# Optimization experiments

Measured on AMD Instinct MI355X. Metric: run time of the kernel, lower is better.

## Reference

```python
import jax, jax.numpy as jnp
import numpy as np

ALPHA = 0.2    # LeakyReLU negative slope (init arg alpha)
HEADS = 8
EPS = 1e-5     # LayerNorm eps


def setup_inputs() -> dict:
    key = jax.random.key(0)
    ks = jax.random.split(key, 16)
    B, S, D = 4, 1024, 256
    dh = D // HEADS  # 32
    x = jax.random.normal(ks[0], (B, S, D), jnp.float32)
    adj = (jax.random.uniform(ks[1], (B, S, S)) < 0.05).astype(jnp.float32)
    adj = jnp.maximum(adj, jnp.eye(S, dtype=jnp.float32)[None])

    def w(k, shape, fan):
        return jax.random.normal(k, shape, jnp.float32) * (fan ** -0.5)

    # GAT layer 0: in->hidden (concat heads)
    W0 = w(ks[2], (D, D), D); a_src0 = w(ks[3], (HEADS, dh), dh); a_dst0 = w(ks[4], (HEADS, dh), dh)
    # GAT layer 1: hidden->hidden (concat heads)
    W1 = w(ks[5], (D, D), D); a_src1 = w(ks[6], (HEADS, dh), dh); a_dst1 = w(ks[7], (HEADS, dh), dh)
    # GAT layer 2: hidden->out (mean over heads, head_dim = out_dim)
    W2 = w(ks[8], (D, HEADS * D), D); a_src2 = w(ks[9], (HEADS, D), D); a_dst2 = w(ks[10], (HEADS, D), D)
    # LayerNorm
    ln_g = jnp.ones((D,), jnp.float32); ln_b = jnp.zeros((D,), jnp.float32)
    # FFN: D -> 2D -> D
    ff_w1 = w(ks[11], (D, 2 * D), D); ff_b1 = jnp.zeros((2 * D,), jnp.float32)
    ff_w2 = w(ks[12], (2 * D, D), 2 * D); ff_b2 = jnp.zeros((D,), jnp.float32)
    return dict(adj=adj, x=x, W0=W0, a_src0=a_src0, a_dst0=a_dst0,
                W1=W1, a_src1=a_src1, a_dst1=a_dst1,
                W2=W2, a_src2=a_src2, a_dst2=a_dst2,
                ln_g=ln_g, ln_b=ln_b,
                ff_w1=ff_w1, ff_b1=ff_b1, ff_w2=ff_w2, ff_b2=ff_b2)


def _gat_layer(h, adj, W, a_src, a_dst, concat):
    B, S, _ = h.shape
    hp = jnp.einsum('bsi,io->bso', h, W).reshape(B, S, HEADS, -1)  # [B,S,H,dh]
    src = jnp.einsum('bshd,hd->bsh', hp, a_src)  # per-node source score
    dst = jnp.einsum('bshd,hd->bsh', hp, a_dst)  # per-node dest score
    # e[b,i,j,h] = LeakyReLU(src_i + dst_j), masked by adjacency
    e = jax.nn.leaky_relu(src[:, :, None, :] + dst[:, None, :, :], ALPHA)
    e = jnp.where(adj[..., None] > 0, e, jnp.float32(-1e9))
    attn = jax.nn.softmax(e, axis=2)  # softmax over neighbors j
    out = jnp.einsum('bijh,bjhd->bihd', attn, hp)
    return out.reshape(B, S, -1) if concat else out.mean(axis=2)


def reference(adj, x, W0, a_src0, a_dst0, W1, a_src1, a_dst1, W2, a_src2, a_dst2,
              ln_g, ln_b, ff_w1, ff_b1, ff_w2, ff_b2):
    # MultiAttentionGAT: 3 layers with residuals, ELU between layers
    h = jax.nn.elu(_gat_layer(x, adj, W0, a_src0, a_dst0, True) + x)
    h = jax.nn.elu(_gat_layer(h, adj, W1, a_src1, a_dst1, True) + h)
    h = _gat_layer(h, adj, W2, a_src2, a_dst2, False) + h
    # LayerNorm
    mu = h.mean(-1, keepdims=True)
    var = h.var(-1, keepdims=True)
    h = (h - mu) * jax.lax.rsqrt(var + EPS) * ln_g + ln_b
    # GELU FFN + residual
    ff = jnp.dot(jax.nn.gelu(jnp.dot(h, ff_w1) + ff_b1), ff_w2) + ff_b2
    return h + ff
```

## Files before the change

### kernel.cpp

```cpp
#include <hip/hip_runtime.h>
#include <hip/hip_bf16.h>

#define B_ 4
#define S_ 1024
#define D_ 256
#define H_ 8
#define LRELU_ALPHA 0.2f
#define MAXDEG 128

typedef __attribute__((ext_vector_type(8))) short short8;
typedef __attribute__((ext_vector_type(4))) float floatx4;

__device__ __forceinline__ float bf2f(unsigned short u) {
    union { unsigned int i; float f; } c; c.i = ((unsigned int)u) << 16; return c.f;
}
__device__ __forceinline__ unsigned short f2bf(float f) {
    union { float f; unsigned int u; } c; c.f = f;
    unsigned int r = (c.u + 0x7FFF + ((c.u >> 16) & 1)) >> 16;
    return (unsigned short)r;
}

__device__ void castT_body(const float* __restrict__ W, unsigned short* __restrict__ out,
                           int K, int N, int k0, int n0, float (*t)[33], int tid) {
    int tx = tid & 31, ty = tid >> 5;
#pragma unroll
    for (int i = 0; i < 4; ++i)
        t[ty + 8 * i][tx] = W[(size_t)(k0 + ty + 8 * i) * N + n0 + tx];
    __syncthreads();
#pragma unroll
    for (int i = 0; i < 4; ++i)
        out[(size_t)(n0 + ty + 8 * i) * K + k0 + tx] = f2bf(t[tx][ty + 8 * i]);
}

__global__ __launch_bounds__(256) void k_prep(
        const float* __restrict__ x, unsigned short* __restrict__ xb,
        const float* __restrict__ W0, unsigned short* __restrict__ W0t,
        const float* __restrict__ W1, unsigned short* __restrict__ W1t,
        const float* __restrict__ W2, unsigned short* __restrict__ W2t,
        const float* __restrict__ F1, unsigned short* __restrict__ F1t,
        const float* __restrict__ F2, unsigned short* __restrict__ F2t,
        const float* __restrict__ as2, const float* __restrict__ ad2,
        float* __restrict__ WS2, float* __restrict__ WD2,
        const float* __restrict__ adj, int* __restrict__ nbr, int* __restrict__ cnt) {
    __shared__ float t[32][33];
    __shared__ int c;
    int b = blockIdx.x, tid = threadIdx.x;
    if (b < 1024) {
        int i = b * 256 + tid;
        float4 v = ((const float4*)x)[i];
        ushort4 u; u.x = f2bf(v.x); u.y = f2bf(v.y); u.z = f2bf(v.z); u.w = f2bf(v.w);
        ((ushort4*)xb)[i] = u;
    } else if (b < 1088) {
        int i = b - 1024; castT_body(W0, W0t, 256, 256, (i & 7) * 32, (i >> 3) * 32, t, tid);
    } else if (b < 1152) {
        int i = b - 1088; castT_body(W1, W1t, 256, 256, (i & 7) * 32, (i >> 3) * 32, t, tid);
    } else if (b < 1664) {
        int i = b - 1152;
        int k0 = (i & 7) * 32, d0 = ((i >> 3) & 7) * 32, h = i >> 6;
        int tx = tid & 31, ty = tid >> 5;
#pragma unroll
        for (int q = 0; q < 4; ++q)
            t[ty + 8 * q][tx] = W2[(size_t)(k0 + ty + 8 * q) * 2048 + h * 256 + d0 + tx];
        __syncthreads();
#pragma unroll
        for (int q = 0; q < 4; ++q)
            W2t[(size_t)(d0 + ty + 8 * q) * 2048 + h * 256 + k0 + tx] = f2bf(t[tx][ty + 8 * q]);
    } else if (b < 1792) {
        int i = b - 1664; castT_body(F1, F1t, 256, 512, (i & 7) * 32, (i >> 3) * 32, t, tid);
    } else if (b < 1920) {
        int i = b - 1792; castT_body(F2, F2t, 512, 256, (i & 15) * 32, (i >> 4) * 32, t, tid);
    } else if (b < 2432) {
        int id = (b - 1920) * 4 + (tid >> 6);
        int h = id >> 8, k = id & 255;
        int lane = tid & 63;
        float4 w4 = *(const float4*)(W2 + (size_t)k * 2048 + h * 256 + lane * 4);
        float4 a4 = *(const float4*)(as2 + h * 256 + lane * 4);
        float4 d4 = *(const float4*)(ad2 + h * 256 + lane * 4);
        float s = w4.x * a4.x + w4.y * a4.y + w4.z * a4.z + w4.w * a4.w;
        float d = w4.x * d4.x + w4.y * d4.y + w4.z * d4.z + w4.w * d4.w;
#pragma unroll
        for (int o = 32; o; o >>= 1) { s += __shfl_xor(s, o); d += __shfl_xor(d, o); }
        if (lane == 0) { WS2[h * 256 + k] = s; WD2[h * 256 + k] = d; }
    } else {
        int row = b - 2432;
        if (tid == 0) c = 0;
        __syncthreads();
        float4 a4 = ((const float4*)(adj + (size_t)row * S_))[tid];
#pragma unroll
        for (int q = 0; q < 4; ++q) {
            float a = q == 0 ? a4.x : q == 1 ? a4.y : q == 2 ? a4.z : a4.w;
            if (a > 0.f) {
                int s = atomicAdd(&c, 1);
                if (s < MAXDEG) nbr[row * MAXDEG + s] = tid * 4 + q;
            }
        }
        __syncthreads();
        if (tid == 0) cnt[row] = c < MAXDEG ? c : MAXDEG;
    }
}

__global__ __launch_bounds__(256) void k_gemm_wide(const unsigned short* __restrict__ A,
        const unsigned short* __restrict__ Bt, float* __restrict__ P,
        int M, int N, int K, int Kc) {
    __shared__ unsigned short As[64][40];
    __shared__ unsigned short Bs[256][40];
    int tid = threadIdx.x;
    int bm = blockIdx.y * 64, bn = blockIdx.x * 256;
    int kbeg = blockIdx.z * Kc, kend = kbeg + Kc;
    int lane = tid & 63, wv = tid >> 6;
    int lrow = lane & 15, lq = lane >> 4;
    floatx4 acc[4][4] = {};
    int sm = tid >> 2, skq = (tid & 3) * 8;
    const unsigned short* Ap = A + (size_t)(bm + sm) * K + skq;
    const unsigned short* Bp0 = Bt + (size_t)(bn + sm) * K + skq;
    const unsigned short* Bp1 = Bp0 + (size_t)64 * K;
    const unsigned short* Bp2 = Bp0 + (size_t)128 * K;
    const unsigned short* Bp3 = Bp0 + (size_t)192 * K;
    short8 av  = *(const short8*)(Ap + kbeg);
    short8 bv0 = *(const short8*)(Bp0 + kbeg);
    short8 bv1 = *(const short8*)(Bp1 + kbeg);
    short8 bv2 = *(const short8*)(Bp2 + kbeg);
    short8 bv3 = *(const short8*)(Bp3 + kbeg);
    for (int k0 = kbeg; k0 < kend; k0 += 32) {
        *(short8*)&As[sm][skq]        = av;
        *(short8*)&Bs[sm][skq]        = bv0;
        *(short8*)&Bs[sm + 64][skq]   = bv1;
        *(short8*)&Bs[sm + 128][skq]  = bv2;
        *(short8*)&Bs[sm + 192][skq]  = bv3;
        __syncthreads();
        if (k0 + 32 < kend) {
            av  = *(const short8*)(Ap + k0 + 32);
            bv0 = *(const short8*)(Bp0 + k0 + 32);
            bv1 = *(const short8*)(Bp1 + k0 + 32);
            bv2 = *(const short8*)(Bp2 + k0 + 32);
            bv3 = *(const short8*)(Bp3 + k0 + 32);
        }
        short8 aF[4], bF[4];
#pragma unroll
        for (int mi = 0; mi < 4; ++mi)
            aF[mi] = *(const short8*)&As[mi * 16 + lrow][lq * 8];
#pragma unroll
        for (int ni = 0; ni < 4; ++ni)
            bF[ni] = *(const short8*)&Bs[wv * 64 + ni * 16 + lrow][lq * 8];
#pragma unroll
        for (int mi = 0; mi < 4; ++mi)
#pragma unroll
            for (int ni = 0; ni < 4; ++ni)
                acc[mi][ni] = __builtin_amdgcn_mfma_f32_16x16x32_bf16(aF[mi], bF[ni], acc[mi][ni], 0, 0, 0);
        __syncthreads();
    }
    float* out = P + (size_t)blockIdx.z * M * N;
#pragma unroll
    for (int mi = 0; mi < 4; ++mi)
#pragma unroll
        for (int ni = 0; ni < 4; ++ni)
#pragma unroll
            for (int r = 0; r < 4; ++r) {
                int grow = bm + mi * 16 + lq * 4 + r;
                int gcol = bn + wv * 64 + ni * 16 + lrow;
                out[(size_t)grow * N + gcol] = acc[mi][ni][r];
            }
}

__global__ __launch_bounds__(256) void k_gemm64s(
        const unsigned short* __restrict__ A, const unsigned short* __restrict__ Bt,
        int N, int K,
        unsigned short* __restrict__ Ob,
        const float* __restrict__ p1, const float* __restrict__ p2,
        float* __restrict__ SRC, float* __restrict__ DST) {
    __shared__ unsigned short As[2][64][40];
    __shared__ unsigned short Bs[2][64][40];
    int tid = threadIdx.x;
    int bm = blockIdx.y * 64, bn = blockIdx.x * 64;
    int lane = tid & 63, wv = tid >> 6;
    int lrow = lane & 15, lq = lane >> 4;
    floatx4 acc[4] = {};
    int sm = tid >> 2, skq = (tid & 3) * 8;
    const unsigned short* Ap = A + (size_t)(bm + sm) * K + skq;
    const unsigned short* Bp = Bt + (size_t)(bn + sm) * K + skq;
    short8 av = *(const short8*)Ap;
    short8 bv = *(const short8*)Bp;
    *(short8*)&As[0][sm][skq] = av;
    *(short8*)&Bs[0][sm][skq] = bv;
    __syncthreads();
    int cur = 0;
    for (int k0 = 0; k0 < K; k0 += 32) {
        bool more = k0 + 32 < K;
        if (more) {
            av = *(const short8*)(Ap + k0 + 32);
            bv = *(const short8*)(Bp + k0 + 32);
        }
        short8 aF = *(const short8*)&As[cur][wv * 16 + lrow][lq * 8];
        short8 bF[4];
#pragma unroll
        for (int ni = 0; ni < 4; ++ni)
            bF[ni] = *(const short8*)&Bs[cur][ni * 16 + lrow][lq * 8];
#pragma unroll
        for (int ni = 0; ni < 4; ++ni)
            acc[ni] = __builtin_amdgcn_mfma_f32_16x16x32_bf16(aF, bF[ni], acc[ni], 0, 0, 0);
        if (more) {
            *(short8*)&As[cur ^ 1][sm][skq] = av;
            *(short8*)&Bs[cur ^ 1][sm][skq] = bv;
            __syncthreads();
            cur ^= 1;
        }
    }
    int row0 = bm + wv * 16 + lq * 4;
#pragma unroll
    for (int ni = 0; ni < 4; ++ni)
#pragma unroll
        for (int r = 0; r < 4; ++r)
            Ob[(size_t)(row0 + r) * N + bn + ni * 16 + lrow] = f2bf(acc[ni][r]);
    float asv[4], adv[4];
#pragma unroll
    for (int ni = 0; ni < 4; ++ni) {
        asv[ni] = p1[bn + ni * 16 + lrow];
        adv[ni] = p2[bn + ni * 16 + lrow];
    }
#pragma unroll
    for (int r = 0; r < 4; ++r) {
        float sA = acc[0][r] * asv[0] + acc[1][r] * asv[1];
        float sB = acc[2][r] * asv[2] + acc[3][r] * asv[3];
        float dA = acc[0][r] * adv[0] + acc[1][r] * adv[1];
        float dB = acc[2][r] * adv[2] + acc[3][r] * adv[3];
#pragma unroll
        for (int o = 8; o; o >>= 1) {
            sA += __shfl_xor(sA, o); sB += __shfl_xor(sB, o);
            dA += __shfl_xor(dA, o); dB += __shfl_xor(dB, o);
        }
        if (lrow == 0) {
            int h0 = bn >> 5;
            SRC[(row0 + r) * 8 + h0]     = sA;
            SRC[(row0 + r) * 8 + h0 + 1] = sB;
            DST[(row0 + r) * 8 + h0]     = dA;
            DST[(row0 + r) * 8 + h0 + 1] = dB;
        }
    }
}

__global__ __launch_bounds__(256) void k_attn4(const unsigned short* __restrict__ hp,
        const float* __restrict__ src, const float* __restrict__ dst,
        const int* __restrict__ nbr, const int* __restrict__ cnts,
        const float* __restrict__ X, float* __restrict__ Hout,
        unsigned short* __restrict__ Hb,
        const float* __restrict__ WS2, const float* __restrict__ WD2,
        float* __restrict__ SRC2, float* __restrict__ DST2) {
    int tid = threadIdx.x;
    int rq = tid >> 6;
    int lane = tid & 63;
    int row = blockIdx.x * 4 + rq;
    int rb = row & ~(S_ - 1);
    __shared__ int nb[4][MAXDEG];
    __shared__ float ew[4][MAXDEG * 9];
    int cnt = cnts[row];
    for (int t = lane; t < cnt; t += 64) nb[rq][t] = nbr[row * MAXDEG + t];
    float4 sa = *(const float4*)(src + row * H_);
    float4 sb = *(const float4*)(src + row * H_ + 4);
    for (int n = lane; n < cnt; n += 64) {
        int j = nb[rq][n];
        const float* dp = dst + (size_t)(rb + j) * H_;
        float4 da = *(const float4*)dp;
        float4 db = *(const float4*)(dp + 4);
        float e;
        e = sa.x + da.x; ew[rq][n * 9 + 0] = e > 0.f ? e : LRELU_ALPHA * e;
        e = sa.y + da.y; ew[rq][n * 9 + 1] = e > 0.f ? e : LRELU_ALPHA * e;
        e = sa.z + da.z; ew[rq][n * 9 + 2] = e > 0.f ? e : LRELU_ALPHA * e;
        e = sa.w + da.w; ew[rq][n * 9 + 3] = e > 0.f ? e : LRELU_ALPHA * e;
        e = sb.x + db.x; ew[rq][n * 9 + 4] = e > 0.f ? e : LRELU_ALPHA * e;
        e = sb.y + db.y; ew[rq][n * 9 + 5] = e > 0.f ? e : LRELU_ALPHA * e;
        e = sb.z + db.z; ew[rq][n * 9 + 6] = e > 0.f ? e : LRELU_ALPHA * e;
        e = sb.w + db.w; ew[rq][n * 9 + 7] = e > 0.f ? e : LRELU_ALPHA * e;
    }
    {
        int h = lane >> 3, s8 = lane & 7;
        float m = -1e30f;
        for (int n = s8; n < cnt; n += 8) m = fmaxf(m, ew[rq][n * 9 + h]);
#pragma unroll
        for (int o = 4; o; o >>= 1) m = fmaxf(m, __shfl_xor(m, o));
        float s = 0.f;
        for (int n = s8; n < cnt; n += 8) {
            float v = __expf(ew[rq][n * 9 + h] - m); ew[rq][n * 9 + h] = v; s += v;
        }
#pragma unroll
        for (int o = 4; o; o >>= 1) s += __shfl_xor(s, o);
        float inv = s > 0.f ? 1.f / s : 0.f;
        for (int n = s8; n < cnt; n += 8) ew[rq][n * 9 + h] *= inv;
    }
    int d0 = lane * 4;
    int h = lane >> 3;
    const unsigned short* hpb = hp + (size_t)rb * 256 + d0;
    const float* ewr = ew[rq];
    float A0 = 0.f, A1 = 0.f, A2 = 0.f, A3 = 0.f;
    float B0 = 0.f, B1 = 0.f, B2 = 0.f, B3 = 0.f;
    int n = 0;
    for (; n + 3 < cnt; n += 4) {
        int j0 = nb[rq][n], j1 = nb[rq][n + 1];
        int j2 = nb[rq][n + 2], j3 = nb[rq][n + 3];
        uint2 p0 = *(const uint2*)(hpb + (size_t)j0 * 256);
        uint2 p1 = *(const uint2*)(hpb + (size_t)j1 * 256);
        uint2 p2 = *(const uint2*)(hpb + (size_t)j2 * 256);
        uint2 p3 = *(const uint2*)(hpb + (size_t)j3 * 256);
        float w0 = ewr[n * 9 + h], w1 = ewr[(n + 1) * 9 + h];
        float w2 = ewr[(n + 2) * 9 + h], w3 = ewr[(n + 3) * 9 + h];
        A0 += w0 * bf2f((unsigned short)p0.x); A1 += w0 * bf2f((unsigned short)(p0.x >> 16));
        A2 += w0 * bf2f((unsigned short)p0.y); A3 += w0 * bf2f((unsigned short)(p0.y >> 16));
        B0 += w1 * bf2f((unsigned short)p1.x); B1 += w1 * bf2f((unsigned short)(p1.x >> 16));
        B2 += w1 * bf2f((unsigned short)p1.y); B3 += w1 * bf2f((unsigned short)(p1.y >> 16));
        A0 += w2 * bf2f((unsigned short)p2.x); A1 += w2 * bf2f((unsigned short)(p2.x >> 16));
        A2 += w2 * bf2f((unsigned short)p2.y); A3 += w2 * bf2f((unsigned short)(p2.y >> 16));
        B0 += w3 * bf2f((unsigned short)p3.x); B1 += w3 * bf2f((unsigned short)(p3.x >> 16));
        B2 += w3 * bf2f((unsigned short)p3.y); B3 += w3 * bf2f((unsigned short)(p3.y >> 16));
    }
    for (; n < cnt; ++n) {
        int j = nb[rq][n];
        uint2 p = *(const uint2*)(hpb + (size_t)j * 256);
        float w = ewr[n * 9 + h];
        A0 += w * bf2f((unsigned short)p.x); A1 += w * bf2f((unsigned short)(p.x >> 16));
        A2 += w * bf2f((unsigned short)p.y); A3 += w * bf2f((unsigned short)(p.y >> 16));
    }
    float4 xv = *(const float4*)(X + (size_t)row * 256 + d0);
    float ov0 = A0 + B0 + xv.x;
    float ov1 = A1 + B1 + xv.y;
    float ov2 = A2 + B2 + xv.z;
    float ov3 = A3 + B3 + xv.w;
    ov0 = ov0 > 0.f ? ov0 : (__expf(ov0) - 1.f);
    ov1 = ov1 > 0.f ? ov1 : (__expf(ov1) - 1.f);
    ov2 = ov2 > 0.f ? ov2 : (__expf(ov2) - 1.f);
    ov3 = ov3 > 0.f ? ov3 : (__expf(ov3) - 1.f);
    *(float4*)(Hout + (size_t)row * 256 + d0) = make_float4(ov0, ov1, ov2, ov3);
    ushort4 ub; ub.x = f2bf(ov0); ub.y = f2bf(ov1); ub.z = f2bf(ov2); ub.w = f2bf(ov3);
    *(ushort4*)(Hb + (size_t)row * 256 + d0) = ub;
    if (WS2 != nullptr) {
#pragma unroll
        for (int hh = 0; hh < 8; ++hh) {
            float4 wsv = *(const float4*)(WS2 + hh * 256 + d0);
            float4 wdv = *(const float4*)(WD2 + hh * 256 + d0);
            float sP = ov0 * wsv.x + ov1 * wsv.y + ov2 * wsv.z + ov3 * wsv.w;
            float dP = ov0 * wdv.x + ov1 * wdv.y + ov2 * wdv.z + ov3 * wdv.w;
#pragma unroll
            for (int o = 32; o; o >>= 1) { sP += __shfl_xor(sP, o); dP += __shfl_xor(dP, o); }
            if (lane == 0) { SRC2[row * 8 + hh] = sP; DST2[row * 8 + hh] = dP; }
        }
    }
}

__global__ __launch_bounds__(256) void k_attn_Y(const unsigned short* __restrict__ Hb,
        const float* __restrict__ src2, const float* __restrict__ dst2,
        const int* __restrict__ nbr, const int* __restrict__ cnts,
        unsigned short* __restrict__ Ycat) {
    int tid = threadIdx.x;
    int half = tid >> 7, sub = tid & 127;
    int row = blockIdx.x * 2 + half;
    int rb = row & ~(S_ - 1);
    __shared__ int nb[2][MAXDEG];
    __shared__ float ew[2][MAXDEG * 8];
    int cnt = cnts[row];
    for (int t = sub; t < cnt; t += 128) nb[half][t] = nbr[row * MAXDEG + t];
    float4 sa = *(const float4*)(src2 + row * H_);
    float4 sb = *(const float4*)(src2 + row * H_ + 4);
    __syncthreads();
    for (int n = sub; n < cnt; n += 128) {
        int j = nb[half][n];
        const float* dp = dst2 + (size_t)(rb + j) * H_;
        float4 da = *(const float4*)dp;
        float4 db = *(const float4*)(dp + 4);
        float e;
        e = sa.x + da.x; ew[half][n * 8 + 0] = e > 0.f ? e : LRELU_ALPHA * e;
        e = sa.y + da.y; ew[half][n * 8 + 1] = e > 0.f ? e : LRELU_ALPHA * e;
        e = sa.z + da.z; ew[half][n * 8 + 2] = e > 0.f ? e : LRELU_ALPHA * e;
        e = sa.w + da.w; ew[half][n * 8 + 3] = e > 0.f ? e : LRELU_ALPHA * e;
        e = sb.x + db.x; ew[half][n * 8 + 4] = e > 0.f ? e : LRELU_ALPHA * e;
        e = sb.y + db.y; ew[half][n * 8 + 5] = e > 0.f ? e : LRELU_ALPHA * e;
        e = sb.z + db.z; ew[half][n * 8 + 6] = e > 0.f ? e : LRELU_ALPHA * e;
        e = sb.w + db.w; ew[half][n * 8 + 7] = e > 0.f ? e : LRELU_ALPHA * e;
    }
    __syncthreads();
    {
        int h = sub >> 4, s16 = sub & 15;
        float m = -1e30f;
        for (int n = s16; n < cnt; n += 16) m = fmaxf(m, ew[half][n * 8 + h]);
#pragma unroll
        for (int o = 8; o; o >>= 1) m = fmaxf(m, __shfl_xor(m, o));
        float s = 0.f;
        for (int n = s16; n < cnt; n += 16) {
            float v = __expf(ew[half][n * 8 + h] - m); ew[half][n * 8 + h] = v; s += v;
        }
#pragma unroll
        for (int o = 8; o; o >>= 1) s += __shfl_xor(s, o);
        float inv = s > 0.f ? 0.125f / s : 0.f;
        for (int n = s16; n < cnt; n += 16) ew[half][n * 8 + h] *= inv;
    }
    __syncthreads();
    const unsigned short* hbase = Hb + (size_t)rb * 256 + 2 * sub;
    const float* ewh = ew[half];
    float aA[8] = {}, aB[8] = {};
    int n = 0;
    for (; n + 1 < cnt; n += 2) {
        int j0 = nb[half][n], j1 = nb[half][n + 1];
        unsigned int p0 = *(const unsigned int*)(hbase + (size_t)j0 * 256);
        unsigned int p1 = *(const unsigned int*)(hbase + (size_t)j1 * 256);
        float4 w0a = *(const float4*)(ewh + n * 8);
        float4 w0b = *(const float4*)(ewh + n * 8 + 4);
        float4 w1a = *(const float4*)(ewh + (n + 1) * 8);
        float4 w1b = *(const float4*)(ewh + (n + 1) * 8 + 4);
        float v0a = bf2f((unsigned short)p0), v0b = bf2f((unsigned short)(p0 >> 16));
        float v1a = bf2f((unsigned short)p1), v1b = bf2f((unsigned short)(p1 >> 16));
        aA[0] += w0a.x * v0a + w1a.x * v1a;  aB[0] += w0a.x * v0b + w1a.x * v1b;
        aA[1] += w0a.y * v0a + w1a.y * v1a;  aB[1] += w0a.y * v0b + w1a.y * v1b;
        aA[2] += w0a.z * v0a + w1a.z * v1a;  aB[2] += w0a.z * v0b + w1a.z * v1b;
        aA[3] += w0a.w * v0a + w1a.w * v1a;  aB[3] += w0a.w * v0b + w1a.w * v1b;
        aA[4] += w0b.x * v0a + w1b.x * v1a;  aB[4] += w0b.x * v0b + w1b.x * v1b;
        aA[5] += w0b.y * v0a + w1b.y * v1a;  aB[5] += w0b.y * v0b + w1b.y * v1b;
        aA[6] += w0b.z * v0a + w1b.z * v1a;  aB[6] += w0b.z * v0b + w1b.z * v1b;
        aA[7] += w0b.w * v0a + w1b.w * v1a;  aB[7] += w0b.w * v0b + w1b.w * v1b;
    }
    for (; n < cnt; ++n) {
        int j = nb[half][n];
        unsigned int p = *(const unsigned int*)(hbase + (size_t)j * 256);
        float4 wa = *(const float4*)(ewh + n * 8);
        float4 wb = *(const float4*)(ewh + n * 8 + 4);
        float va = bf2f((unsigned short)p), vb = bf2f((unsigned short)(p >> 16));
        aA[0] += wa.x * va; aB[0] += wa.x * vb;
        aA[1] += wa.y * va; aB[1] += wa.y * vb;
        aA[2] += wa.z * va; aB[2] += wa.z * vb;
        aA[3] += wa.w * va; aB[3] += wa.w * vb;
        aA[4] += wb.x * va; aB[4] += wb.x * vb;
        aA[5] += wb.y * va; aB[5] += wb.y * vb;
        aA[6] += wb.z * va; aB[6] += wb.z * vb;
        aA[7] += wb.w * va; aB[7] += wb.w * vb;
    }
    unsigned short* yb = Ycat + (size_t)row * 2048 + 2 * sub;
#pragma unroll
    for (int hh = 0; hh < 8; ++hh) {
        ushort2 u; u.x = f2bf(aA[hh]); u.y = f2bf(aB[hh]);
        *(ushort2*)(yb + hh * 256) = u;
    }
}

__global__ __launch_bounds__(512) void k_tail3(
        const float* __restrict__ PP, const float* __restrict__ Hres,
        const float* __restrict__ g, const float* __restrict__ bta,
        const unsigned short* __restrict__ F1t, const float* __restrict__ b1,
        const unsigned short* __restrict__ F2t, const float* __restrict__ b2,
        float* __restrict__ out) {
    __shared__ unsigned short alnb[16][264];
    __shared__ unsigned short mid[16][520];
    __shared__ unsigned short Bs[2][256][36];
    int tid = threadIdx.x;
    int lane = tid & 63, wv = tid >> 6;
    int lrow = lane & 15, lq = lane >> 4;
    int r0 = blockIdx.x * 16;

    float4 gg = ((const float4*)g)[lane];
    float4 bbv = ((const float4*)bta)[lane];
#pragma unroll
    for (int pass = 0; pass < 2; ++pass) {
        int lr = wv * 2 + pass;
        int row = r0 + lr;
        float4 v = ((const float4*)(Hres + (size_t)row * 256))[lane];
#pragma unroll
        for (int sp = 0; sp < 8; ++sp) {
            float4 p = ((const float4*)(PP + (size_t)sp * 1048576 + (size_t)row * 256))[lane];
            v.x += p.x; v.y += p.y; v.z += p.z; v.w += p.w;
        }
        float s = v.x + v.y + v.z + v.w;
        float q = v.x * v.x + v.y * v.y + v.z * v.z + v.w * v.w;
#pragma unroll
        for (int o = 32; o; o >>= 1) { s += __shfl_xor(s, o); q += __shfl_xor(q, o); }
        float mu = s * (1.f / 256.f);
        float var = q * (1.f / 256.f) - mu * mu;
        if (var < 0.f) var = 0.f;
        float rs = rsqrtf(var + 1e-5f);
        ushort4 ub;
        ub.x = f2bf((v.x - mu) * rs * gg.x + bbv.x);
        ub.y = f2bf((v.y - mu) * rs * gg.y + bbv.y);
        ub.z = f2bf((v.z - mu) * rs * gg.z + bbv.z);
        ub.w = f2bf((v.w - mu) * rs * gg.w + bbv.w);
        *(ushort4*)&alnb[lr][lane * 4] = ub;
    }
    __syncthreads();

    int sm = tid >> 1, skq = (tid & 1) * 16;
    int colb = wv * 32 + lrow;

#pragma unroll 1
    for (int hf = 0; hf < 2; ++hf) {
        floatx4 acc1[2] = {};
        const unsigned short* Fp = F1t + (size_t)(hf * 256 + sm) * 256 + skq;
        short8 rb0 = *(const short8*)Fp;
        short8 rb1 = *(const short8*)(Fp + 8);
        __syncthreads();
        *(short8*)&Bs[0][sm][skq]     = rb0;
        *(short8*)&Bs[0][sm][skq + 8] = rb1;
        __syncthreads();
        int cur = 0;
        for (int st = 0; st < 8; ++st) {
            bool more = st < 7;
            if (more) {
                rb0 = *(const short8*)(Fp + (st + 1) * 32);
                rb1 = *(const short8*)(Fp + (st + 1) * 32 + 8);
            }
            int k0 = st * 32;
            short8 aF  = *(const short8*)&alnb[lrow][k0 + lq * 8];
            short8 bF0 = *(const short8*)&Bs[cur][wv * 32 + lrow][lq * 8];
            short8 bF1 = *(const short8*)&Bs[cur][wv * 32 + 16 + lrow][lq * 8];
            acc1[0] = __builtin_amdgcn_mfma_f32_16x16x32_bf16(aF, bF0, acc1[0], 0, 0, 0);
            acc1[1] = __builtin_amdgcn_mfma_f32_16x16x32_bf16(aF, bF1, acc1[1], 0, 0, 0);
            if (more) {
                *(short8*)&Bs[cur ^ 1][sm][skq]     = rb0;
                *(short8*)&Bs[cur ^ 1][sm][skq + 8] = rb1;
                __syncthreads();
                cur ^= 1;
            }
        }
#pragma unroll
        for (int ni = 0; ni < 2; ++ni) {
            int gcol = hf * 256 + colb + ni * 16;
            float bb = b1[gcol];
#pragma unroll
            for (int r = 0; r < 4; ++r) {
                float xx = acc1[ni][r] + bb;
                float tt = tanhf(0.7978845608028654f * (xx + 0.044715f * xx * xx * xx));
                mid[lq * 4 + r][gcol] = f2bf(0.5f * xx * (1.f + tt));
            }
        }
    }
    __syncthreads();

    floatx4 acc2[2] = {};
    const unsigned short* F2p = F2t + (size_t)sm * 512 + skq;
    short8 rc0 = *(const short8*)F2p;
    short8 rc1 = *(const short8*)(F2p + 8);
    *(short8*)&Bs[0][sm][skq]     = rc0;
    *(short8*)&Bs[0][sm][skq + 8] = rc1;
    __syncthreads();
    int cur = 0;
    for (int st = 0; st < 16; ++st) {
        bool more = st < 15;
        if (more) {
            rc0 = *(const short8*)(F2p + (st + 1) * 32);
            rc1 = *(const short8*)(F2p + (st + 1) * 32 + 8);
        }
        int k0 = st * 32;
        short8 aF  = *(const short8*)&mid[lrow][k0 + lq * 8];
        short8 bF0 = *(const short8*)&Bs[cur][wv * 32 + lrow][lq * 8];
        short8 bF1 = *(const short8*)&Bs[cur][wv * 32 + 16 + lrow][lq * 8];
        acc2[0] = __builtin_amdgcn_mfma_f32_16x16x32_bf16(aF, bF0, acc2[0], 0, 0, 0);
        acc2[1] = __builtin_amdgcn_mfma_f32_16x16x32_bf16(aF, bF1, acc2[1], 0, 0, 0);
        if (more) {
            *(short8*)&Bs[cur ^ 1][sm][skq]     = rc0;
            *(short8*)&Bs[cur ^ 1][sm][skq + 8] = rc1;
            __syncthreads();
            cur ^= 1;
        }
    }
#pragma unroll
    for (int ni = 0; ni < 2; ++ni) {
        int col = colb + ni * 16;
        float bb = b2[col];
#pragma unroll
        for (int r = 0; r < 4; ++r) {
            int lr = lq * 4 + r;
            float res = bf2f(alnb[lr][col]);
            out[(size_t)(r0 + lr) * 256 + col] = acc2[ni][r] + bb + res;
        }
    }
}

extern "C" void kernel_launch(void* const* d_in, const int* in_sizes, int n_in,
                              void* d_out, int out_size, void* d_ws, size_t ws_size,
                              hipStream_t stream) {
    const float* adj   = (const float*)d_in[0];
    const float* x     = (const float*)d_in[1];
    const float* W0    = (const float*)d_in[2];
    const float* as0   = (const float*)d_in[3];
    const float* ad0   = (const float*)d_in[4];
    const float* W1    = (const float*)d_in[5];
    const float* as1   = (const float*)d_in[6];
    const float* ad1   = (const float*)d_in[7];
    const float* W2    = (const float*)d_in[8];
    const float* as2   = (const float*)d_in[9];
    const float* ad2   = (const float*)d_in[10];
    const float* ln_g  = (const float*)d_in[11];
    const float* ln_b  = (const float*)d_in[12];
    const float* ff_w1 = (const float*)d_in[13];
    const float* ff_b1 = (const float*)d_in[14];
    const float* ff_w2 = (const float*)d_in[15];
    const float* ff_b2 = (const float*)d_in[16];

    float* ws = (float*)d_ws;
    float* H    = ws;
    unsigned short* Ycat = (unsigned short*)(ws + 2097152);
    unsigned short* HPb  = (unsigned short*)(ws + 6291456);
    unsigned short* xb   = (unsigned short*)(ws + 6815744);
    unsigned short* Hb   = (unsigned short*)(ws + 7340032);
    unsigned short* W0t  = (unsigned short*)(ws + 9437184);
    unsigned short* W1t  = (unsigned short*)(ws + 9469952);
    unsigned short* W2t  = (unsigned short*)(ws + 9502720);
    unsigned short* F1t  = (unsigned short*)(ws + 9764864);
    unsigned short* F2t  = (unsigned short*)(ws + 9830400);
    float* WS2  = ws + 9895936;
    float* WD2  = ws + 9897984;
    float* SRC  = ws + 9900032;
    float* DST  = ws + 9932800;
    float* SRC2 = ws + 9965568;
    float* DST2 = ws + 9998336;
    int*   NBR  = (int*)(ws + 10031104);
    int*   CNT  = (int*)(ws + 10555392);
    float* PP   = ws + 12582912;

    k_prep<<<6528, 256, 0, stream>>>(x, xb, W0, W0t, W1, W1t, W2, W2t,
                                     ff_w1, F1t, ff_w2, F2t, as2, ad2, WS2, WD2,
                                     adj, NBR, CNT);

    k_gemm64s<<<dim3(4, 64), 256, 0, stream>>>(xb, W0t, 256, 256, HPb, as0, ad0, SRC, DST);
    k_attn4<<<1024, 256, 0, stream>>>(HPb, SRC, DST, NBR, CNT, x, H, Hb,
                                      nullptr, nullptr, nullptr, nullptr);

    k_gemm64s<<<dim3(4, 64), 256, 0, stream>>>(Hb, W1t, 256, 256, HPb, as1, ad1, SRC, DST);
    k_attn4<<<1024, 256, 0, stream>>>(HPb, SRC, DST, NBR, CNT, H, H, Hb,
                                      WS2, WD2, SRC2, DST2);

    k_attn_Y<<<2048, 256, 0, stream>>>(Hb, SRC2, DST2, NBR, CNT, Ycat);
    k_gemm_wide<<<dim3(1, 64, 8), 256, 0, stream>>>(Ycat, W2t, PP, 4096, 256, 2048, 256);

    k_tail3<<<256, 512, 0, stream>>>(PP, H, ln_g, ln_b, F1t, ff_b1, F2t, ff_b2,
                                     (float*)d_out);
}
```

Baseline: 209.5 us.

## Double-buffer LDS in wide GEMM and split neighbor gather across half-waves

The wide GEMM now keeps two LDS stages, so the next K-slice is stored into the alternate buffer after the MFMAs. This drops one barrier per iteration and overlaps the global loads with compute, at the cost of doubling shared memory per block. The attention aggregation kernel now has each lane gather 8 bf16 values (16-byte loads), with the two half-waves handling alternating neighbors and combining partial sums by shuffle. This widens memory transactions and adds memory-level parallelism per row, but only half the lanes do the output writes.

```diff
diff --git a/kernel.cpp b/kernel.cpp
--- a/kernel.cpp
+++ b/kernel.cpp
@@ -102,8 +102,8 @@
 __global__ __launch_bounds__(256) void k_gemm_wide(const unsigned short* __restrict__ A,
         const unsigned short* __restrict__ Bt, float* __restrict__ P,
         int M, int N, int K, int Kc) {
-    __shared__ unsigned short As[64][40];
-    __shared__ unsigned short Bs[256][40];
+    __shared__ unsigned short As[2][64][40];
+    __shared__ unsigned short Bs[2][256][40];
     int tid = threadIdx.x;
     int bm = blockIdx.y * 64, bn = blockIdx.x * 256;
     int kbeg = blockIdx.z * Kc, kend = kbeg + Kc;
@@ -121,14 +121,16 @@
     short8 bv1 = *(const short8*)(Bp1 + kbeg);
     short8 bv2 = *(const short8*)(Bp2 + kbeg);
     short8 bv3 = *(const short8*)(Bp3 + kbeg);
+    *(short8*)&As[0][sm][skq]        = av;
+    *(short8*)&Bs[0][sm][skq]        = bv0;
+    *(short8*)&Bs[0][sm + 64][skq]   = bv1;
+    *(short8*)&Bs[0][sm + 128][skq]  = bv2;
+    *(short8*)&Bs[0][sm + 192][skq]  = bv3;
+    __syncthreads();
+    int cur = 0;
     for (int k0 = kbeg; k0 < kend; k0 += 32) {
-        *(short8*)&As[sm][skq]        = av;
-        *(short8*)&Bs[sm][skq]        = bv0;
-        *(short8*)&Bs[sm + 64][skq]   = bv1;
-        *(short8*)&Bs[sm + 128][skq]  = bv2;
-        *(short8*)&Bs[sm + 192][skq]  = bv3;
-        __syncthreads();
-        if (k0 + 32 < kend) {
+        bool more = k0 + 32 < kend;
+        if (more) {
             av  = *(const short8*)(Ap + k0 + 32);
             bv0 = *(const short8*)(Bp0 + k0 + 32);
             bv1 = *(const short8*)(Bp1 + k0 + 32);
@@ -138,16 +140,24 @@
         short8 aF[4], bF[4];
 #pragma unroll
         for (int mi = 0; mi < 4; ++mi)
-            aF[mi] = *(const short8*)&As[mi * 16 + lrow][lq * 8];
+            aF[mi] = *(const short8*)&As[cur][mi * 16 + lrow][lq * 8];
 #pragma unroll
         for (int ni = 0; ni < 4; ++ni)
-            bF[ni] = *(const short8*)&Bs[wv * 64 + ni * 16 + lrow][lq * 8];
+            bF[ni] = *(const short8*)&Bs[cur][wv * 64 + ni * 16 + lrow][lq * 8];
 #pragma unroll
         for (int mi = 0; mi < 4; ++mi)
 #pragma unroll
             for (int ni = 0; ni < 4; ++ni)
                 acc[mi][ni] = __builtin_amdgcn_mfma_f32_16x16x32_bf16(aF[mi], bF[ni], acc[mi][ni], 0, 0, 0);
-        __syncthreads();
+        if (more) {
+            *(short8*)&As[cur ^ 1][sm][skq]        = av;
+            *(short8*)&Bs[cur ^ 1][sm][skq]        = bv0;
+            *(short8*)&Bs[cur ^ 1][sm + 64][skq]   = bv1;
+            *(short8*)&Bs[cur ^ 1][sm + 128][skq]  = bv2;
+            *(short8*)&Bs[cur ^ 1][sm + 192][skq]  = bv3;
+            __syncthreads();
+            cur ^= 1;
+        }
     }
     float* out = P + (size_t)blockIdx.z * M * N;
 #pragma unroll
@@ -286,57 +296,70 @@
         float inv = s > 0.f ? 1.f / s : 0.f;
         for (int n = s8; n < cnt; n += 8) ew[rq][n * 9 + h] *= inv;
     }
-    int d0 = lane * 4;
-    int h = lane >> 3;
+    int half = lane >> 5, sl = lane & 31;
+    int d0 = sl * 8;
+    int h = sl >> 2;
     const unsigned short* hpb = hp + (size_t)rb * 256 + d0;
     const float* ewr = ew[rq];
-    float A0 = 0.f, A1 = 0.f, A2 = 0.f, A3 = 0.f;
-    float B0 = 0.f, B1 = 0.f, B2 = 0.f, B3 = 0.f;
-    int n = 0;
-    for (; n + 3 < cnt; n += 4) {
-        int j0 = nb[rq][n], j1 = nb[rq][n + 1];
-        int j2 = nb[rq][n + 2], j3 = nb[rq][n + 3];
-        uint2 p0 = *(const uint2*)(hpb + (size_t)j0 * 256);
-        uint2 p1 = *(const uint2*)(hpb + (size_t)j1 * 256);
-        uint2 p2 = *(const uint2*)(hpb + (size_t)j2 * 256);
-        uint2 p3 = *(const uint2*)(hpb + (size_t)j3 * 256);
-        float w0 = ewr[n * 9 + h], w1 = ewr[(n + 1) * 9 + h];
-        float w2 = ewr[(n + 2) * 9 + h], w3 = ewr[(n + 3) * 9 + h];
-        A0 += w0 * bf2f((unsigned short)p0.x); A1 += w0 * bf2f((unsigned short)(p0.x >> 16));
-        A2 += w0 * bf2f((unsigned short)p0.y); A3 += w0 * bf2f((unsigned short)(p0.y >> 16));
-        B0 += w1 * bf2f((unsigned short)p1.x); B1 += w1 * bf2f((unsigned short)(p1.x >> 16));
-        B2 += w1 * bf2f((unsigned short)p1.y); B3 += w1 * bf2f((unsigned short)(p1.y >> 16));
-        A0 += w2 * bf2f((unsigned short)p2.x); A1 += w2 * bf2f((unsigned short)(p2.x >> 16));
-        A2 += w2 * bf2f((unsigned short)p2.y); A3 += w2 * bf2f((unsigned short)(p2.y >> 16));
-        B0 += w3 * bf2f((unsigned short)p3.x); B1 += w3 * bf2f((unsigned short)(p3.x >> 16));
-        B2 += w3 * bf2f((unsigned short)p3.y); B3 += w3 * bf2f((unsigned short)(p3.y >> 16));
-    }
-    for (; n < cnt; ++n) {
+    float aA[8] = {}, aB[8] = {};
+    int n = half;
+    for (; n + 2 < cnt; n += 4) {
+        int j0 = nb[rq][n], j1 = nb[rq][n + 2];
+        uint4 p0 = *(const uint4*)(hpb + (size_t)j0 * 256);
+        uint4 p1 = *(const uint4*)(hpb + (size_t)j1 * 256);
+        float w0 = ewr[n * 9 + h], w1 = ewr[(n + 2) * 9 + h];
+        aA[0] += w0 * bf2f((unsigned short)p0.x); aA[1] += w0 * bf2f((unsigned short)(p0.x >> 16));
+        aA[2] += w0 * bf2f((unsigned short)p0.y); aA[3] += w0 * bf2f((unsigned short)(p0.y >> 16));
+        aA[4] += w0 * bf2f((unsigned short)p0.z); aA[5] += w0 * bf2f((unsigned short)(p0.z >> 16));
+        aA[6] += w0 * bf2f((unsigned short)p0.w); aA[7] += w0 * bf2f((unsigned short)(p0.w >> 16));
+        aB[0] += w1 * bf2f((unsigned short)p1.x); aB[1] += w1 * bf2f((unsigned short)(p1.x >> 16));
+        aB[2] += w1 * bf2f((unsigned short)p1.y); aB[3] += w1 * bf2f((unsigned short)(p1.y >> 16));
+        aB[4] += w1 * bf2f((unsigned short)p1.z); aB[5] += w1 * bf2f((unsigned short)(p1.z >> 16));
+        aB[6] += w1 * bf2f((unsigned short)p1.w); aB[7] += w1 * bf2f((unsigned short)(p1.w >> 16));
+    }
+    for (; n < cnt; n += 2) {
         int j = nb[rq][n];
-        uint2 p = *(const uint2*)(hpb + (size_t)j * 256);
+        uint4 p = *(const uint4*)(hpb + (size_t)j * 256);
         float w = ewr[n * 9 + h];
-        A0 += w * bf2f((unsigned short)p.x); A1 += w * bf2f((unsigned short)(p.x >> 16));
-        A2 += w * bf2f((unsigned short)p.y); A3 += w * bf2f((unsigned short)(p.y >> 16));
-    }
-    float4 xv = *(const float4*)(X + (size_t)row * 256 + d0);
-    float ov0 = A0 + B0 + xv.x;
-    float ov1 = A1 + B1 + xv.y;
-    float ov2 = A2 + B2 + xv.z;
-    float ov3 = A3 + B3 + xv.w;
-    ov0 = ov0 > 0.f ? ov0 : (__expf(ov0) - 1.f);
-    ov1 = ov1 > 0.f ? ov1 : (__expf(ov1) - 1.f);
-    ov2 = ov2 > 0.f ? ov2 : (__expf(ov2) - 1.f);
-    ov3 = ov3 > 0.f ? ov3 : (__expf(ov3) - 1.f);
-    *(float4*)(Hout + (size_t)row * 256 + d0) = make_float4(ov0, ov1, ov2, ov3);
-    ushort4 ub; ub.x = f2bf(ov0); ub.y = f2bf(ov1); ub.z = f2bf(ov2); ub.w = f2bf(ov3);
-    *(ushort4*)(Hb + (size_t)row * 256 + d0) = ub;
+        aA[0] += w * bf2f((unsigned short)p.x); aA[1] += w * bf2f((unsigned short)(p.x >> 16));
+        aA[2] += w * bf2f((unsigned short)p.y); aA[3] += w * bf2f((unsigned short)(p.y >> 16));
+        aA[4] += w * bf2f((unsigned short)p.z); aA[5] += w * bf2f((unsigned short)(p.z >> 16));
+        aA[6] += w * bf2f((unsigned short)p.w); aA[7] += w * bf2f((unsigned short)(p.w >> 16));
+    }
+    float ov[8];
+#pragma unroll
+    for (int i = 0; i < 8; ++i) {
+        float s = aA[i] + aB[i];
+        s += __shfl_xor(s, 32);
+        ov[i] = s;
+    }
+    float4 xv0 = *(const float4*)(X + (size_t)row * 256 + d0);
+    float4 xv1 = *(const float4*)(X + (size_t)row * 256 + d0 + 4);
+    ov[0] += xv0.x; ov[1] += xv0.y; ov[2] += xv0.z; ov[3] += xv0.w;
+    ov[4] += xv1.x; ov[5] += xv1.y; ov[6] += xv1.z; ov[7] += xv1.w;
+#pragma unroll
+    for (int i = 0; i < 8; ++i) ov[i] = ov[i] > 0.f ? ov[i] : (__expf(ov[i]) - 1.f);
+    if (half == 0) {
+        *(float4*)(Hout + (size_t)row * 256 + d0)     = make_float4(ov[0], ov[1], ov[2], ov[3]);
+        *(float4*)(Hout + (size_t)row * 256 + d0 + 4) = make_float4(ov[4], ov[5], ov[6], ov[7]);
+        ushort4 u0, u1;
+        u0.x = f2bf(ov[0]); u0.y = f2bf(ov[1]); u0.z = f2bf(ov[2]); u0.w = f2bf(ov[3]);
+        u1.x = f2bf(ov[4]); u1.y = f2bf(ov[5]); u1.z = f2bf(ov[6]); u1.w = f2bf(ov[7]);
+        *(ushort4*)(Hb + (size_t)row * 256 + d0)     = u0;
+        *(ushort4*)(Hb + (size_t)row * 256 + d0 + 4) = u1;
+    }
     if (WS2 != nullptr) {
+        float msk = half ? 0.f : 1.f;
 #pragma unroll
         for (int hh = 0; hh < 8; ++hh) {
-            float4 wsv = *(const float4*)(WS2 + hh * 256 + d0);
-            float4 wdv = *(const float4*)(WD2 + hh * 256 + d0);
-            float sP = ov0 * wsv.x + ov1 * wsv.y + ov2 * wsv.z + ov3 * wsv.w;
-            float dP = ov0 * wdv.x + ov1 * wdv.y + ov2 * wdv.z + ov3 * wdv.w;
+            float4 w0 = *(const float4*)(WS2 + hh * 256 + d0);
+            float4 w1 = *(const float4*)(WS2 + hh * 256 + d0 + 4);
+            float4 v0 = *(const float4*)(WD2 + hh * 256 + d0);
+            float4 v1 = *(const float4*)(WD2 + hh * 256 + d0 + 4);
+            float sP = msk * (ov[0] * w0.x + ov[1] * w0.y + ov[2] * w0.z + ov[3] * w0.w
+                            + ov[4] * w1.x + ov[5] * w1.y + ov[6] * w1.z + ov[7] * w1.w);
+            float dP = msk * (ov[0] * v0.x + ov[1] * v0.y + ov[2] * v0.z + ov[3] * v0.w
+                            + ov[4] * v1.x + ov[5] * v1.y + ov[6] * v1.z + ov[7] * v1.w);
 #pragma unroll
             for (int o = 32; o; o >>= 1) { sP += __shfl_xor(sP, o); dP += __shfl_xor(dP, o); }
             if (lane == 0) { SRC2[row * 8 + hh] = sP; DST2[row * 8 + hh] = dP; }
```

Measured after the change: 214.9 us. 1.03x slower.
